# Performance work log

Measured on AMD Instinct MI355X. Metric: run time of the kernel, lower is better.

Reference implementation:

```python
import jax, jax.numpy as jnp
import numpy as np


def _hippo_scale_params(N, L):
    """Replicates HiPPOScale.__init__ for discretization='bilinear' (pure numpy)."""
    q = np.arange(N, dtype=np.float64)
    col, row = np.meshgrid(q, q)
    r = 2 * q + 1
    M = -(np.where(row >= col, r, 0) - np.diag(q))
    T = np.sqrt(np.diag(2 * q + 1))
    A = T @ M @ np.linalg.inv(T)          # (N, N)
    B = np.diag(T)                         # (N,)
    ts = np.arange(1, L + 1, dtype=np.float64)[:, None, None]  # (L,1,1)
    At = A[None] / ts                      # A / t, batched over t
    I = np.eye(N, dtype=np.float64)
    Mm = I[None] - 0.5 * At
    Nn = I[None] + 0.5 * At
    A_stacked = np.linalg.solve(Mm, Nn)                      # (L, N, N)
    Bt = B[None, :] / ts[:, 0, :]                             # (L, N)
    B_stacked = np.linalg.solve(Mm, Bt[..., None])[..., 0]    # (L, N)
    return A_stacked.astype(np.float32), B_stacked.astype(np.float32)


def setup_inputs() -> dict:
    N, L, Bsz = 64, 4096, 64
    key = jax.random.key(0)
    A_st, B_st = _hippo_scale_params(N, L)
    inputs = jax.random.normal(key, (L, Bsz), dtype=jnp.float32)
    return {
        "inputs": inputs,                       # (L, B)
        "A_stacked": jnp.asarray(A_st),         # (L, N, N)
        "B_stacked": jnp.asarray(B_st),         # (L, N)
    }


def reference(inputs, A_stacked, B_stacked):
    # u[t, b, :] = inputs[t, b] * B_stacked[t, :]   -> (L, B, N)
    u = inputs[..., None] * B_stacked[:, None, :]

    # x[t] = A[t] @ x[t-1] + u[t], x[-1] = 0  (time-varying linear recurrence).
    # The torch code computes this via a divide-and-conquer unroll; here we use
    # the equivalent parallel associative scan with elements (A, u) and
    # composition (A2@A1, A2@u1 + u2).
    def combine(e1, e2):
        a1, u1 = e1
        a2, u2 = e2
        a = jnp.matmul(a2, a1)                                  # (l, N, N)
        v = jnp.einsum('...ij,...bj->...bi', a2, u1) + u2       # (l, B, N)
        return (a, v)

    _, x = jax.lax.associative_scan(combine, (A_stacked, u))
    return x  # (L, B, N)
```

## Files before the change

kernel.cpp:

```cpp
#include <hip/hip_runtime.h>
#include <hip/hip_bf16.h>

#define TL 4096
#define NB 64
#define CH 8
#define CN 512
#define AS 72

typedef __attribute__((ext_vector_type(8))) short short8;
typedef __attribute__((ext_vector_type(4))) short short4v;
typedef __attribute__((ext_vector_type(4))) float floatx4;
typedef __attribute__((ext_vector_type(4))) unsigned int uint4v;

__device__ inline floatx4 mfma_bf16(short8 a, short8 b, floatx4 c) {
    return __builtin_amdgcn_mfma_f32_16x16x32_bf16(a, b, c, 0, 0, 0);
}
__device__ inline short bf16_rne(float x) {
    union { __hip_bfloat16 b; unsigned short s; } u;
    u.b = __float2bfloat16(x);
    return (short)u.s;
}
__device__ inline void split_bf16(float x, short& h, short& l) {
    h = bf16_rne(x);
    union { unsigned u; float f; } hv; hv.u = ((unsigned)(unsigned short)h) << 16;
    l = bf16_rne(x - hv.f);
}
__device__ inline void cvt_frag(float4 a, float4 b, short8& H, short8& L) {
    float v[8] = {a.x,a.y,a.z,a.w,b.x,b.y,b.z,b.w};
#pragma unroll
    for (int r = 0; r < 8; ++r) { short hh,ll; split_bf16(v[r],hh,ll); H[r]=hh; L[r]=ll; }
}
__device__ inline void unpack_frag(uint4v a, uint4v b, short8& H, short8& L) {
#pragma unroll
    for (int r = 0; r < 4; ++r) {
        H[r]   = (short)(a[r] >> 16); L[r]   = (short)(a[r] & 0xFFFFu);
        H[4+r] = (short)(b[r] >> 16); L[4+r] = (short)(b[r] & 0xFFFFu);
    }
}

__global__ __launch_bounds__(256, 2)
void hippo_phase1(const float* __restrict__ inp, const float* __restrict__ Ag,
                  const float* __restrict__ Bst,
                  unsigned* __restrict__ P32, float* __restrict__ VT)
{
    __shared__ short SBh[2][NB][AS], SBl[2][NB][AS];
    __shared__ short VBh[2][NB][AS], VBl[2][NB][AS];

    const int tid = threadIdx.x;
    const int c = blockIdx.x, t0 = c * CH;
    const int w = tid >> 6, lane = tid & 63;
    const int quad = lane >> 4, l15 = lane & 15;
    const int arow = 16*w + l15;
    const int wr0  = 16*w + 4*quad;

    float4 rA[2][2];
#pragma unroll
    for (int kc = 0; kc < 2; ++kc) {
        const float* p = Ag + (size_t)(t0+1)*4096 + (size_t)arow*64 + 32*kc + 8*quad;
        rA[kc][0] = *(const float4*)p;
        rA[kc][1] = *(const float4*)(p + 4);
    }
    float4 bnxt = *(const float4*)(Bst + (size_t)(t0+1)*64 + wr0);
    float inxt[4];
#pragma unroll
    for (int ni = 0; ni < 4; ++ni) inxt[ni] = inp[(size_t)(t0+1)*64 + l15 + 16*ni];

    floatx4 accS[4], accV[4];
    {
        const float* A0 = Ag + (size_t)t0 * 4096;
        float4 b0 = *(const float4*)(Bst + (size_t)t0*64 + wr0);
        float bc[4] = {b0.x,b0.y,b0.z,b0.w};
#pragma unroll
        for (int ni = 0; ni < 4; ++ni) {
            const float ii = inp[(size_t)t0*64 + l15 + 16*ni];
#pragma unroll
            for (int r = 0; r < 4; ++r) {
                accS[ni][r] = A0[(size_t)(wr0 + r)*64 + l15 + 16*ni];
                accV[ni][r] = bc[r] * ii;
            }
        }
    }
#pragma unroll
    for (int ni = 0; ni < 4; ++ni) {
        const int cc = l15 + 16*ni;
        short4v h4, l4;
#pragma unroll
        for (int r = 0; r < 4; ++r) { short hh,ll; split_bf16(accS[ni][r],hh,ll); h4[r]=hh; l4[r]=ll; }
        *(short4v*)&SBh[0][cc][wr0] = h4; *(short4v*)&SBl[0][cc][wr0] = l4;
#pragma unroll
        for (int r = 0; r < 4; ++r) { short hh,ll; split_bf16(accV[ni][r],hh,ll); h4[r]=hh; l4[r]=ll; }
        *(short4v*)&VBh[0][cc][wr0] = h4; *(short4v*)&VBl[0][cc][wr0] = l4;
    }
    __syncthreads();

    short8 aH[2], aL[2];
#pragma unroll
    for (int kc = 0; kc < 2; ++kc) cvt_frag(rA[kc][0], rA[kc][1], aH[kc], aL[kc]);

    int cur = 0;
    float4 bcur = bnxt;
    float icur[4];
#pragma unroll
    for (int ni = 0; ni < 4; ++ni) icur[ni] = inxt[ni];

    for (int s = 1; s < CH; ++s) {
        if (s + 1 < CH) {
            const int t1 = t0 + s + 1;
#pragma unroll
            for (int kc = 0; kc < 2; ++kc) {
                const float* p = Ag + (size_t)t1*4096 + (size_t)arow*64 + 32*kc + 8*quad;
                rA[kc][0] = *(const float4*)p;
                rA[kc][1] = *(const float4*)(p + 4);
            }
            bnxt = *(const float4*)(Bst + (size_t)t1*64 + wr0);
#pragma unroll
            for (int ni = 0; ni < 4; ++ni) inxt[ni] = inp[(size_t)t1*64 + l15 + 16*ni];
        }
        {
            float bc[4] = {bcur.x,bcur.y,bcur.z,bcur.w};
#pragma unroll
            for (int ni = 0; ni < 4; ++ni)
#pragma unroll
            for (int r = 0; r < 4; ++r) {
                accS[ni][r] = 0.0f;
                accV[ni][r] = bc[r] * icur[ni];
            }
        }
#pragma unroll
        for (int kc = 0; kc < 2; ++kc) {
            const int ko = 32*kc + 8*quad;
#pragma unroll
            for (int ni = 0; ni < 4; ++ni) {
                const int n = l15 + 16*ni;
                short8 sH = *(const short8*)&SBh[cur][n][ko];
                short8 sL = *(const short8*)&SBl[cur][n][ko];
                short8 vH = *(const short8*)&VBh[cur][n][ko];
                short8 vL = *(const short8*)&VBl[cur][n][ko];
                accS[ni] = mfma_bf16(aH[kc], sH, accS[ni]);
                accS[ni] = mfma_bf16(aH[kc], sL, accS[ni]);
                accS[ni] = mfma_bf16(aL[kc], sH, accS[ni]);
                accV[ni] = mfma_bf16(aH[kc], vH, accV[ni]);
                accV[ni] = mfma_bf16(aH[kc], vL, accV[ni]);
                accV[ni] = mfma_bf16(aL[kc], vH, accV[ni]);
            }
        }
        if (s + 1 < CH) {
#pragma unroll
            for (int kc = 0; kc < 2; ++kc) cvt_frag(rA[kc][0], rA[kc][1], aH[kc], aL[kc]);
            const int nb = cur ^ 1;
#pragma unroll
            for (int ni = 0; ni < 4; ++ni) {
                const int cc = l15 + 16*ni;
                short4v h4, l4;
#pragma unroll
                for (int r = 0; r < 4; ++r) { short hh,ll; split_bf16(accS[ni][r],hh,ll); h4[r]=hh; l4[r]=ll; }
                *(short4v*)&SBh[nb][cc][wr0] = h4; *(short4v*)&SBl[nb][cc][wr0] = l4;
#pragma unroll
                for (int r = 0; r < 4; ++r) { short hh,ll; split_bf16(accV[ni][r],hh,ll); h4[r]=hh; l4[r]=ll; }
                *(short4v*)&VBh[nb][cc][wr0] = h4; *(short4v*)&VBl[nb][cc][wr0] = l4;
            }
            __syncthreads();
            cur ^= 1;
        }
        bcur = bnxt;
#pragma unroll
        for (int ni = 0; ni < 4; ++ni) icur[ni] = inxt[ni];
    }

    unsigned* po = P32 + (size_t)c * 4096;
#pragma unroll
    for (int ni = 0; ni < 4; ++ni) {
        const int cc = l15 + 16*ni;
        *(floatx4*)(VT + (size_t)c*4096 + cc*64 + wr0) = accV[ni];
#pragma unroll
        for (int r = 0; r < 4; ++r) {
            short hh, ll; split_bf16(accS[ni][r], hh, ll);
            po[(size_t)(wr0 + r)*64 + cc] = ((unsigned)(unsigned short)hh << 16) | (unsigned)(unsigned short)ll;
        }
    }
}

__global__ __launch_bounds__(256, 2)
void hippo_seqscan(unsigned* __restrict__ P32, float* __restrict__ VT,
                   int bstride, int off0, int estride)
{
    __shared__ short PBh[2][NB][AS], PBl[2][NB][AS];
    __shared__ short VBh[2][NB][AS], VBl[2][NB][AS];

    const int tid = threadIdx.x;
    const int base = blockIdx.x * bstride + off0;
    const int w = tid >> 6, lane = tid & 63;
    const int quad = lane >> 4, l15 = lane & 15;
    const int arow = 16*w + l15;
    const int wr0  = 16*w + 4*quad;

    {
        const unsigned* p0 = P32 + (size_t)base * 4096;
        const float*    v0 = VT  + (size_t)base * 4096;
#pragma unroll
        for (int q = 0; q < 4; ++q) {
            int f = tid + q * 256;
            int k = f & 63, m0 = (f >> 6) * 4;
            uint4v pk = *(const uint4v*)(p0 + k * 64 + m0);
#pragma unroll
            for (int r = 0; r < 4; ++r) {
                PBh[0][m0 + r][k] = (short)(pk[r] >> 16);
                PBl[0][m0 + r][k] = (short)(pk[r] & 0xFFFFu);
            }
        }
#pragma unroll
        for (int q = 0; q < 4; ++q) {
            int f = tid + q * 256;
            int n = f >> 4, k0 = (f & 15) * 4;
            float4 vv = *(const float4*)(v0 + n * 64 + k0);
            float va[4] = {vv.x, vv.y, vv.z, vv.w};
            short4v vh4, vl4;
#pragma unroll
            for (int r = 0; r < 4; ++r) { short hh, ll; split_bf16(va[r], hh, ll); vh4[r]=hh; vl4[r]=ll; }
            *(short4v*)&VBh[0][n][k0] = vh4; *(short4v*)&VBl[0][n][k0] = vl4;
        }
    }
    uint4v rP[2][2]; float4 preV[4];
    {
        const unsigned* pc = P32 + (size_t)(base + estride) * 4096;
        const float*    vc = VT  + (size_t)(base + estride) * 4096;
#pragma unroll
        for (int kc = 0; kc < 2; ++kc) {
            const unsigned* p = pc + (size_t)arow*64 + 32*kc + 8*quad;
            rP[kc][0] = *(const uint4v*)p;
            rP[kc][1] = *(const uint4v*)(p + 4);
        }
#pragma unroll
        for (int ni = 0; ni < 4; ++ni)
            preV[ni] = *(const float4*)(vc + (size_t)(l15 + 16*ni)*64 + wr0);
    }
    __syncthreads();

    short8 aH[2], aL[2];
#pragma unroll
    for (int kc = 0; kc < 2; ++kc) unpack_frag(rP[kc][0], rP[kc][1], aH[kc], aL[kc]);

    int cur = 0;
    for (int i = 1; i < 8; ++i) {
        const int idx = base + i * estride;
        floatx4 accP[4], accV[4];
#pragma unroll
        for (int ni = 0; ni < 4; ++ni) {
            accV[ni][0] = preV[ni].x; accV[ni][1] = preV[ni].y;
            accV[ni][2] = preV[ni].z; accV[ni][3] = preV[ni].w;
            accP[ni][0]=accP[ni][1]=accP[ni][2]=accP[ni][3]=0.0f;
        }
        if (i + 1 < 8) {
            const unsigned* pc = P32 + (size_t)(base + (i+1) * estride) * 4096;
            const float*    vc = VT  + (size_t)(base + (i+1) * estride) * 4096;
#pragma unroll
            for (int kc = 0; kc < 2; ++kc) {
                const unsigned* p = pc + (size_t)arow*64 + 32*kc + 8*quad;
                rP[kc][0] = *(const uint4v*)p;
                rP[kc][1] = *(const uint4v*)(p + 4);
            }
#pragma unroll
            for (int ni = 0; ni < 4; ++ni)
                preV[ni] = *(const float4*)(vc + (size_t)(l15 + 16*ni)*64 + wr0);
        }
#pragma unroll
        for (int kc = 0; kc < 2; ++kc) {
            const int ko = 32*kc + 8*quad;
#pragma unroll
            for (int ni = 0; ni < 4; ++ni) {
                const int n = l15 + 16*ni;
                short8 pH = *(const short8*)&PBh[cur][n][ko];
                short8 pL = *(const short8*)&PBl[cur][n][ko];
                short8 vH = *(const short8*)&VBh[cur][n][ko];
                short8 vL = *(const short8*)&VBl[cur][n][ko];
                accP[ni] = mfma_bf16(aH[kc], pH, accP[ni]);
                accP[ni] = mfma_bf16(aH[kc], pL, accP[ni]);
                accP[ni] = mfma_bf16(aL[kc], pH, accP[ni]);
                accV[ni] = mfma_bf16(aH[kc], vH, accV[ni]);
                accV[ni] = mfma_bf16(aH[kc], vL, accV[ni]);
                accV[ni] = mfma_bf16(aL[kc], vH, accV[ni]);
            }
        }
        if (i + 1 < 8) {
#pragma unroll
            for (int kc = 0; kc < 2; ++kc) unpack_frag(rP[kc][0], rP[kc][1], aH[kc], aL[kc]);
        }
        unsigned* po = P32 + (size_t)idx * 4096;
        const int nb = cur ^ 1;
#pragma unroll
        for (int ni = 0; ni < 4; ++ni) {
            const int cc = l15 + 16*ni;
            *(floatx4*)(VT + (size_t)idx*4096 + cc*64 + wr0) = accV[ni];
            short4v h4, l4;
#pragma unroll
            for (int r = 0; r < 4; ++r) {
                short hh, ll; split_bf16(accP[ni][r], hh, ll);
                po[(size_t)(wr0+r)*64 + cc] = ((unsigned)(unsigned short)hh << 16) | (unsigned)(unsigned short)ll;
                h4[r]=hh; l4[r]=ll;
            }
            if (i + 1 < 8) {
                *(short4v*)&PBh[nb][cc][wr0] = h4; *(short4v*)&PBl[nb][cc][wr0] = l4;
                short4v vh4, vl4;
#pragma unroll
                for (int r = 0; r < 4; ++r) { short hh,ll; split_bf16(accV[ni][r],hh,ll); vh4[r]=hh; vl4[r]=ll; }
                *(short4v*)&VBh[nb][cc][wr0] = vh4; *(short4v*)&VBl[nb][cc][wr0] = vl4;
            }
        }
        if (i + 1 < 8) __syncthreads();
        cur ^= 1;
    }
}

__global__ __launch_bounds__(256, 2)
void hippo_s3(unsigned* __restrict__ P32, const float* __restrict__ VT)
{
    __shared__ short EBh[2][NB][AS], EBl[2][NB][AS];
    const int tid = threadIdx.x;
    const int w = tid >> 6, lane = tid & 63, quad = lane >> 4, l15 = lane & 15;
    const int arow = 16*w + l15;
    const int wr0  = 16*w + 4*quad;

#pragma unroll
    for (int q = 0; q < 16; ++q) {
        int f = tid + q * 256; EBh[0][f >> 6][f & 63] = 0; EBl[0][f >> 6][f & 63] = 0;
    }
    uint4v rP[2][2]; float4 preV[4];
    {
        const unsigned* pc = P32 + (size_t)63 * 4096;
        const float*    vc = VT  + (size_t)63 * 4096;
#pragma unroll
        for (int kc = 0; kc < 2; ++kc) {
            const unsigned* p = pc + (size_t)arow*64 + 32*kc + 8*quad;
            rP[kc][0] = *(const uint4v*)p;
            rP[kc][1] = *(const uint4v*)(p + 4);
        }
#pragma unroll
        for (int ni = 0; ni < 4; ++ni)
            preV[ni] = *(const float4*)(vc + (size_t)(l15 + 16*ni)*64 + wr0);
    }
    __syncthreads();

    short8 aH[2], aL[2];
#pragma unroll
    for (int kc = 0; kc < 2; ++kc) unpack_frag(rP[kc][0], rP[kc][1], aH[kc], aL[kc]);

    int cur = 0;
    for (int s = 0; s < 7; ++s) {
        const int idx = 64 * s + 63;
        floatx4 acc[4];
#pragma unroll
        for (int ni = 0; ni < 4; ++ni) {
            acc[ni][0] = preV[ni].x; acc[ni][1] = preV[ni].y;
            acc[ni][2] = preV[ni].z; acc[ni][3] = preV[ni].w;
        }
        if (s + 1 < 7) {
            const int idx2 = 64 * (s + 1) + 63;
            const unsigned* pc = P32 + (size_t)idx2 * 4096;
            const float*    vc = VT  + (size_t)idx2 * 4096;
#pragma unroll
            for (int kc = 0; kc < 2; ++kc) {
                const unsigned* p = pc + (size_t)arow*64 + 32*kc + 8*quad;
                rP[kc][0] = *(const uint4v*)p;
                rP[kc][1] = *(const uint4v*)(p + 4);
            }
#pragma unroll
            for (int ni = 0; ni < 4; ++ni)
                preV[ni] = *(const float4*)(vc + (size_t)(l15 + 16*ni)*64 + wr0);
        }
#pragma unroll
        for (int kc = 0; kc < 2; ++kc) {
            const int ko = 32*kc + 8*quad;
#pragma unroll
            for (int ni = 0; ni < 4; ++ni) {
                const int n = l15 + 16*ni;
                short8 eH = *(const short8*)&EBh[cur][n][ko];
                short8 eL = *(const short8*)&EBl[cur][n][ko];
                acc[ni] = mfma_bf16(aH[kc], eH, acc[ni]);
                acc[ni] = mfma_bf16(aH[kc], eL, acc[ni]);
                acc[ni] = mfma_bf16(aL[kc], eH, acc[ni]);
            }
        }
        if (s + 1 < 7) {
#pragma unroll
            for (int kc = 0; kc < 2; ++kc) unpack_frag(rP[kc][0], rP[kc][1], aH[kc], aL[kc]);
        }
        float* eo = (float*)(P32 + (size_t)idx * 4096);
        const int nb = cur ^ 1;
#pragma unroll
        for (int ni = 0; ni < 4; ++ni) {
            const int cc = l15 + 16*ni;
            *(floatx4*)(eo + cc*64 + wr0) = acc[ni];
            if (s + 1 < 7) {
                short4v h4, l4;
#pragma unroll
                for (int r = 0; r < 4; ++r) { short hh,ll; split_bf16(acc[ni][r],hh,ll); h4[r]=hh; l4[r]=ll; }
                *(short4v*)&EBh[nb][cc][wr0] = h4; *(short4v*)&EBl[nb][cc][wr0] = l4;
            }
        }
        if (s + 1 < 7) __syncthreads();
        cur ^= 1;
    }
}

__global__ __launch_bounds__(256, 2)
void hippo_phase3(const float* __restrict__ inp, const float* __restrict__ Ag,
                  const float* __restrict__ Bst, const unsigned* __restrict__ P32,
                  const float* __restrict__ VT, float* __restrict__ out)
{
    __shared__ short XBh[2][NB][AS], XBl[2][NB][AS];

    const int tid = threadIdx.x, c = blockIdx.x, t0 = c * CH;
    const int w = tid >> 6, lane = tid & 63, quad = lane >> 4, l15 = lane & 15;
    const int arow = 16*w + l15;
    const int wr0  = 16*w + 4*quad;
    const int sup = c >> 6, g = c >> 3, gi = g & 7, j = c & 7;

    float4 rA[2][2];
#pragma unroll
    for (int kc = 0; kc < 2; ++kc) {
        const float* p = Ag + (size_t)t0*4096 + (size_t)arow*64 + 32*kc + 8*quad;
        rA[kc][0] = *(const float4*)p;
        rA[kc][1] = *(const float4*)(p + 4);
    }
    float4 bcur = *(const float4*)(Bst + (size_t)t0*64 + wr0);
    float icur[4];
#pragma unroll
    for (int ni = 0; ni < 4; ++ni) icur[ni] = inp[(size_t)t0*64 + l15 + 16*ni];

    if (sup == 0) {
#pragma unroll
        for (int q = 0; q < 16; ++q) { int f = tid + q*256; XBh[0][f>>6][f&63] = 0; XBl[0][f>>6][f&63] = 0; }
    } else {
        const float* e = (const float*)(P32 + (size_t)(64*(sup-1) + 63) * 4096);
#pragma unroll
        for (int q = 0; q < 4; ++q) {
            int f = tid + q*256; int b = f>>4, k0 = (f&15)*4;
            float4 v = *(const float4*)(e + b*64 + k0);
            float va[4] = {v.x,v.y,v.z,v.w};
            short4v h4, l4;
#pragma unroll
            for (int r=0;r<4;++r){short hh,ll;split_bf16(va[r],hh,ll);h4[r]=hh;l4[r]=ll;}
            *(short4v*)&XBh[0][b][k0] = h4; *(short4v*)&XBl[0][b][k0] = l4;
        }
    }
    __syncthreads();
    int cur = 0;

    auto combine = [&](int idx) {
        uint4v rP[2][2];
        const unsigned* pc = P32 + (size_t)idx * 4096;
        const float*    vc = VT  + (size_t)idx * 4096;
#pragma unroll
        for (int kc = 0; kc < 2; ++kc) {
            const unsigned* p = pc + (size_t)arow*64 + 32*kc + 8*quad;
            rP[kc][0] = *(const uint4v*)p;
            rP[kc][1] = *(const uint4v*)(p + 4);
        }
        floatx4 acc[4];
#pragma unroll
        for (int ni = 0; ni < 4; ++ni) {
            float4 vv = *(const float4*)(vc + (size_t)(l15 + 16*ni)*64 + wr0);
            acc[ni][0]=vv.x; acc[ni][1]=vv.y; acc[ni][2]=vv.z; acc[ni][3]=vv.w;
        }
        short8 cH[2], cL[2];
#pragma unroll
        for (int kc = 0; kc < 2; ++kc) unpack_frag(rP[kc][0], rP[kc][1], cH[kc], cL[kc]);
#pragma unroll
        for (int kc = 0; kc < 2; ++kc) {
            const int ko = 32*kc + 8*quad;
#pragma unroll
            for (int ni = 0; ni < 4; ++ni) {
                const int n = l15 + 16*ni;
                short8 xH = *(const short8*)&XBh[cur][n][ko];
                short8 xL = *(const short8*)&XBl[cur][n][ko];
                acc[ni] = mfma_bf16(cH[kc], xH, acc[ni]);
                acc[ni] = mfma_bf16(cH[kc], xL, acc[ni]);
                acc[ni] = mfma_bf16(cL[kc], xH, acc[ni]);
            }
        }
        const int nb = cur ^ 1;
#pragma unroll
        for (int ni = 0; ni < 4; ++ni) {
            const int cc = l15 + 16*ni;
            short4v h4, l4;
#pragma unroll
            for (int r=0;r<4;++r){short hh,ll;split_bf16(acc[ni][r],hh,ll);h4[r]=hh;l4[r]=ll;}
            *(short4v*)&XBh[nb][cc][wr0] = h4; *(short4v*)&XBl[nb][cc][wr0] = l4;
        }
        __syncthreads();
        cur ^= 1;
    };
    if (gi) combine(8*g - 1);
    if (j)  combine(c - 1);

    short8 aH[2], aL[2];
#pragma unroll
    for (int kc = 0; kc < 2; ++kc) cvt_frag(rA[kc][0], rA[kc][1], aH[kc], aL[kc]);

    float4 bnxt; float inxt[4];
    floatx4 acc[4];
    for (int s = 0; s < CH; ++s) {
        const int t = t0 + s;
        if (s + 1 < CH) {
            const int t1 = t + 1;
#pragma unroll
            for (int kc = 0; kc < 2; ++kc) {
                const float* p = Ag + (size_t)t1*4096 + (size_t)arow*64 + 32*kc + 8*quad;
                rA[kc][0] = *(const float4*)p;
                rA[kc][1] = *(const float4*)(p + 4);
            }
            bnxt = *(const float4*)(Bst + (size_t)t1*64 + wr0);
#pragma unroll
            for (int ni = 0; ni < 4; ++ni) inxt[ni] = inp[(size_t)t1*64 + l15 + 16*ni];
        }
        {
            float bc[4] = {bcur.x,bcur.y,bcur.z,bcur.w};
#pragma unroll
            for (int ni=0;ni<4;++ni)
#pragma unroll
            for (int r=0;r<4;++r) acc[ni][r] = bc[r] * icur[ni];
        }
#pragma unroll
        for (int kc = 0; kc < 2; ++kc) {
            const int ko = 32*kc + 8*quad;
#pragma unroll
            for (int ni = 0; ni < 4; ++ni) {
                const int n = l15 + 16*ni;
                short8 xH = *(const short8*)&XBh[cur][n][ko];
                short8 xL = *(const short8*)&XBl[cur][n][ko];
                acc[ni] = mfma_bf16(aH[kc], xH, acc[ni]);
                acc[ni] = mfma_bf16(aH[kc], xL, acc[ni]);
                acc[ni] = mfma_bf16(aL[kc], xH, acc[ni]);
            }
        }
        if (s + 1 < CH) {
#pragma unroll
            for (int kc = 0; kc < 2; ++kc) cvt_frag(rA[kc][0], rA[kc][1], aH[kc], aL[kc]);
        }
        const int nb = cur ^ 1;
#pragma unroll
        for (int ni = 0; ni < 4; ++ni) {
            const int cc = l15 + 16*ni;
            *(floatx4*)(out + (size_t)t*4096 + cc*64 + wr0) = acc[ni];
            if (s + 1 < CH) {
                short4v h4, l4;
#pragma unroll
                for (int r=0;r<4;++r){short hh,ll;split_bf16(acc[ni][r],hh,ll);h4[r]=hh;l4[r]=ll;}
                *(short4v*)&XBh[nb][cc][wr0] = h4; *(short4v*)&XBl[nb][cc][wr0] = l4;
            }
        }
        if (s + 1 < CH) { __syncthreads(); cur ^= 1; }
        bcur = bnxt;
#pragma unroll
        for (int ni = 0; ni < 4; ++ni) icur[ni] = inxt[ni];
    }
}

extern "C" void kernel_launch(void* const* d_in, const int* in_sizes, int n_in,
                              void* d_out, int out_size, void* d_ws, size_t ws_size,
                              hipStream_t stream)
{
    const float* inp = (const float*)d_in[0];
    const float* A   = (const float*)d_in[1];
    const float* Bst = (const float*)d_in[2];
    float* out = (float*)d_out;
    float* ws  = (float*)d_ws;

    unsigned* P32 = (unsigned*)ws;
    float*    VT  = ws + (size_t)CN * 4096;

    hippo_phase1<<<CN, 256, 0, stream>>>(inp, A, Bst, P32, VT);
    hippo_seqscan<<<64, 256, 0, stream>>>(P32, VT, 8, 0, 1);
    hippo_seqscan<<<8, 256, 0, stream>>>(P32, VT, 64, 7, 8);
    hippo_s3<<<1, 256, 0, stream>>>(P32, VT);
    hippo_phase3<<<CN, 256, 0, stream>>>(inp, A, Bst, P32, VT, out);
}
```

Baseline: 183.9 us.

## Fuse five scan kernels into one persistent kernel with grid barriers

Replaces the chain of launches (chunk-local phase, two sequential-scan levels, top-level scan, final expansion) with a single kernel of 512 blocks that synchronise through atomic-counter grid barriers, reusing the same shared-memory buffers across phases. The aim is to remove kernel launch gaps and tail effects between the stages. It depends on all 512 blocks being co-resident (two blocks per CU on 256 CUs), adds a memset for the barrier counters, and leaves most blocks spinning while the small scan stages run.

```diff
diff --git a/kernel.cpp b/kernel.cpp
--- a/kernel.cpp
+++ b/kernel.cpp
@@ -38,13 +38,26 @@
     }
 }
 
+__device__ inline void grid_barrier(unsigned* cnt, unsigned nb) {
+    __threadfence();
+    __syncthreads();
+    if (threadIdx.x == 0) {
+        __hip_atomic_fetch_add(cnt, 1u, __ATOMIC_ACQ_REL, __HIP_MEMORY_SCOPE_AGENT);
+        while (__hip_atomic_load(cnt, __ATOMIC_ACQUIRE, __HIP_MEMORY_SCOPE_AGENT) < nb)
+            __builtin_amdgcn_s_sleep(2);
+    }
+    __syncthreads();
+    __threadfence();
+}
+
 __global__ __launch_bounds__(256, 2)
-void hippo_phase1(const float* __restrict__ inp, const float* __restrict__ Ag,
-                  const float* __restrict__ Bst,
-                  unsigned* __restrict__ P32, float* __restrict__ VT)
+void hippo_fused(const float* __restrict__ inp, const float* __restrict__ Ag,
+                 const float* __restrict__ Bst, unsigned* __restrict__ P32,
+                 float* __restrict__ VT, float* __restrict__ out,
+                 unsigned* __restrict__ gbar)
 {
-    __shared__ short SBh[2][NB][AS], SBl[2][NB][AS];
-    __shared__ short VBh[2][NB][AS], VBl[2][NB][AS];
+    __shared__ short B0h[2][NB][AS], B0l[2][NB][AS];
+    __shared__ short B1h[2][NB][AS], B1l[2][NB][AS];
 
     const int tid = threadIdx.x;
     const int c = blockIdx.x, t0 = c * CH;
@@ -53,206 +66,179 @@
     const int arow = 16*w + l15;
     const int wr0  = 16*w + 4*quad;
 
-    float4 rA[2][2];
+    {
+        float4 rA[2][2];
+#pragma unroll
+        for (int kc = 0; kc < 2; ++kc) {
+            const float* p = Ag + (size_t)(t0+1)*4096 + (size_t)arow*64 + 32*kc + 8*quad;
+            rA[kc][0] = *(const float4*)p;
+            rA[kc][1] = *(const float4*)(p + 4);
+        }
+        float4 bnxt = *(const float4*)(Bst + (size_t)(t0+1)*64 + wr0);
+        float inxt[4];
+#pragma unroll
+        for (int ni = 0; ni < 4; ++ni) inxt[ni] = inp[(size_t)(t0+1)*64 + l15 + 16*ni];
+
+        floatx4 accS[4], accV[4];
+        {
+            const float* A0 = Ag + (size_t)t0 * 4096;
+            float4 b0 = *(const float4*)(Bst + (size_t)t0*64 + wr0);
+            float bc[4] = {b0.x,b0.y,b0.z,b0.w};
+#pragma unroll
+            for (int ni = 0; ni < 4; ++ni) {
+                const float ii = inp[(size_t)t0*64 + l15 + 16*ni];
+#pragma unroll
+                for (int r = 0; r < 4; ++r) {
+                    accS[ni][r] = A0[(size_t)(wr0 + r)*64 + l15 + 16*ni];
+                    accV[ni][r] = bc[r] * ii;
+                }
+            }
+        }
+#pragma unroll
+        for (int ni = 0; ni < 4; ++ni) {
+            const int cc = l15 + 16*ni;
+            short4v h4, l4;
+#pragma unroll
+            for (int r = 0; r < 4; ++r) { short hh,ll; split_bf16(accS[ni][r],hh,ll); h4[r]=hh; l4[r]=ll; }
+            *(short4v*)&B0h[0][cc][wr0] = h4; *(short4v*)&B0l[0][cc][wr0] = l4;
+#pragma unroll
+            for (int r = 0; r < 4; ++r) { short hh,ll; split_bf16(accV[ni][r],hh,ll); h4[r]=hh; l4[r]=ll; }
+            *(short4v*)&B1h[0][cc][wr0] = h4; *(short4v*)&B1l[0][cc][wr0] = l4;
+        }
+        __syncthreads();
+
+        short8 aH[2], aL[2];
+#pragma unroll
+        for (int kc = 0; kc < 2; ++kc) cvt_frag(rA[kc][0], rA[kc][1], aH[kc], aL[kc]);
+
+        int cur = 0;
+        float4 bcur = bnxt;
+        float icur[4];
+#pragma unroll
+        for (int ni = 0; ni < 4; ++ni) icur[ni] = inxt[ni];
+
+        for (int s = 1; s < CH; ++s) {
+            if (s + 1 < CH) {
+                const int t1 = t0 + s + 1;
+#pragma unroll
+                for (int kc = 0; kc < 2; ++kc) {
+                    const float* p = Ag + (size_t)t1*4096 + (size_t)arow*64 + 32*kc + 8*quad;
+                    rA[kc][0] = *(const float4*)p;
+                    rA[kc][1] = *(const float4*)(p + 4);
+                }
+                bnxt = *(const float4*)(Bst + (size_t)t1*64 + wr0);
+#pragma unroll
+                for (int ni = 0; ni < 4; ++ni) inxt[ni] = inp[(size_t)t1*64 + l15 + 16*ni];
+            }
+            {
+                float bc[4] = {bcur.x,bcur.y,bcur.z,bcur.w};
+#pragma unroll
+                for (int ni = 0; ni < 4; ++ni)
+#pragma unroll
+                for (int r = 0; r < 4; ++r) {
+                    accS[ni][r] = 0.0f;
+                    accV[ni][r] = bc[r] * icur[ni];
+                }
+            }
+#pragma unroll
+            for (int kc = 0; kc < 2; ++kc) {
+                const int ko = 32*kc + 8*quad;
+#pragma unroll
+                for (int ni = 0; ni < 4; ++ni) {
+                    const int n = l15 + 16*ni;
+                    short8 sH = *(const short8*)&B0h[cur][n][ko];
+                    short8 sL = *(const short8*)&B0l[cur][n][ko];
+                    short8 vH = *(const short8*)&B1h[cur][n][ko];
+                    short8 vL = *(const short8*)&B1l[cur][n][ko];
+                    accS[ni] = mfma_bf16(aH[kc], sH, accS[ni]);
+                    accS[ni] = mfma_bf16(aH[kc], sL, accS[ni]);
+                    accS[ni] = mfma_bf16(aL[kc], sH, accS[ni]);
+                    accV[ni] = mfma_bf16(aH[kc], vH, accV[ni]);
+                    accV[ni] = mfma_bf16(aH[kc], vL, accV[ni]);
+                    accV[ni] = mfma_bf16(aL[kc], vH, accV[ni]);
+                }
+            }
+            if (s + 1 < CH) {
+#pragma unroll
+                for (int kc = 0; kc < 2; ++kc) cvt_frag(rA[kc][0], rA[kc][1], aH[kc], aL[kc]);
+                const int nb = cur ^ 1;
+#pragma unroll
+                for (int ni = 0; ni < 4; ++ni) {
+                    const int cc = l15 + 16*ni;
+                    short4v h4, l4;
+#pragma unroll
+                    for (int r = 0; r < 4; ++r) { short hh,ll; split_bf16(accS[ni][r],hh,ll); h4[r]=hh; l4[r]=ll; }
+                    *(short4v*)&B0h[nb][cc][wr0] = h4; *(short4v*)&B0l[nb][cc][wr0] = l4;
+#pragma unroll
+                    for (int r = 0; r < 4; ++r) { short hh,ll; split_bf16(accV[ni][r],hh,ll); h4[r]=hh; l4[r]=ll; }
+                    *(short4v*)&B1h[nb][cc][wr0] = h4; *(short4v*)&B1l[nb][cc][wr0] = l4;
+                }
+                __syncthreads();
+                cur ^= 1;
+            }
+            bcur = bnxt;
+#pragma unroll
+            for (int ni = 0; ni < 4; ++ni) icur[ni] = inxt[ni];
+        }
+
+        unsigned* po = P32 + (size_t)c * 4096;
+#pragma unroll
+        for (int ni = 0; ni < 4; ++ni) {
+            const int cc = l15 + 16*ni;
+            *(floatx4*)(VT + (size_t)c*4096 + cc*64 + wr0) = accV[ni];
+#pragma unroll
+            for (int r = 0; r < 4; ++r) {
+                short hh, ll; split_bf16(accS[ni][r], hh, ll);
+                po[(size_t)(wr0 + r)*64 + cc] = ((unsigned)(unsigned short)hh << 16) | (unsigned)(unsigned short)ll;
+            }
+        }
+    }
+
+    float4 rA3[2][2];
 #pragma unroll
     for (int kc = 0; kc < 2; ++kc) {
-        const float* p = Ag + (size_t)(t0+1)*4096 + (size_t)arow*64 + 32*kc + 8*quad;
-        rA[kc][0] = *(const float4*)p;
-        rA[kc][1] = *(const float4*)(p + 4);
+        const float* p = Ag + (size_t)t0*4096 + (size_t)arow*64 + 32*kc + 8*quad;
+        rA3[kc][0] = *(const float4*)p;
+        rA3[kc][1] = *(const float4*)(p + 4);
     }
-    float4 bnxt = *(const float4*)(Bst + (size_t)(t0+1)*64 + wr0);
-    float inxt[4];
-#pragma unroll
-    for (int ni = 0; ni < 4; ++ni) inxt[ni] = inp[(size_t)(t0+1)*64 + l15 + 16*ni];
-
-    floatx4 accS[4], accV[4];
-    {
-        const float* A0 = Ag + (size_t)t0 * 4096;
-        float4 b0 = *(const float4*)(Bst + (size_t)t0*64 + wr0);
-        float bc[4] = {b0.x,b0.y,b0.z,b0.w};
-#pragma unroll
-        for (int ni = 0; ni < 4; ++ni) {
-            const float ii = inp[(size_t)t0*64 + l15 + 16*ni];
-#pragma unroll
-            for (int r = 0; r < 4; ++r) {
-                accS[ni][r] = A0[(size_t)(wr0 + r)*64 + l15 + 16*ni];
-                accV[ni][r] = bc[r] * ii;
-            }
-        }
-    }
-#pragma unroll
-    for (int ni = 0; ni < 4; ++ni) {
-        const int cc = l15 + 16*ni;
-        short4v h4, l4;
-#pragma unroll
-        for (int r = 0; r < 4; ++r) { short hh,ll; split_bf16(accS[ni][r],hh,ll); h4[r]=hh; l4[r]=ll; }
-        *(short4v*)&SBh[0][cc][wr0] = h4; *(short4v*)&SBl[0][cc][wr0] = l4;
-#pragma unroll
-        for (int r = 0; r < 4; ++r) { short hh,ll; split_bf16(accV[ni][r],hh,ll); h4[r]=hh; l4[r]=ll; }
-        *(short4v*)&VBh[0][cc][wr0] = h4; *(short4v*)&VBl[0][cc][wr0] = l4;
-    }
-    __syncthreads();
-
-    short8 aH[2], aL[2];
-#pragma unroll
-    for (int kc = 0; kc < 2; ++kc) cvt_frag(rA[kc][0], rA[kc][1], aH[kc], aL[kc]);
-
-    int cur = 0;
-    float4 bcur = bnxt;
-    float icur[4];
-#pragma unroll
-    for (int ni = 0; ni < 4; ++ni) icur[ni] = inxt[ni];
-
-    for (int s = 1; s < CH; ++s) {
-        if (s + 1 < CH) {
-            const int t1 = t0 + s + 1;
-#pragma unroll
-            for (int kc = 0; kc < 2; ++kc) {
-                const float* p = Ag + (size_t)t1*4096 + (size_t)arow*64 + 32*kc + 8*quad;
-                rA[kc][0] = *(const float4*)p;
-                rA[kc][1] = *(const float4*)(p + 4);
-            }
-            bnxt = *(const float4*)(Bst + (size_t)t1*64 + wr0);
-#pragma unroll
-            for (int ni = 0; ni < 4; ++ni) inxt[ni] = inp[(size_t)t1*64 + l15 + 16*ni];
-        }
+    float4 b3 = *(const float4*)(Bst + (size_t)t0*64 + wr0);
+    float i3[4];
+#pragma unroll
+    for (int ni = 0; ni < 4; ++ni) i3[ni] = inp[(size_t)t0*64 + l15 + 16*ni];
+
+    grid_barrier(gbar + 0, CN);
+
+    auto scan8 = [&](int base, int estride) {
         {
-            float bc[4] = {bcur.x,bcur.y,bcur.z,bcur.w};
-#pragma unroll
-            for (int ni = 0; ni < 4; ++ni)
-#pragma unroll
-            for (int r = 0; r < 4; ++r) {
-                accS[ni][r] = 0.0f;
-                accV[ni][r] = bc[r] * icur[ni];
-            }
-        }
-#pragma unroll
-        for (int kc = 0; kc < 2; ++kc) {
-            const int ko = 32*kc + 8*quad;
-#pragma unroll
-            for (int ni = 0; ni < 4; ++ni) {
-                const int n = l15 + 16*ni;
-                short8 sH = *(const short8*)&SBh[cur][n][ko];
-                short8 sL = *(const short8*)&SBl[cur][n][ko];
-                short8 vH = *(const short8*)&VBh[cur][n][ko];
-                short8 vL = *(const short8*)&VBl[cur][n][ko];
-                accS[ni] = mfma_bf16(aH[kc], sH, accS[ni]);
-                accS[ni] = mfma_bf16(aH[kc], sL, accS[ni]);
-                accS[ni] = mfma_bf16(aL[kc], sH, accS[ni]);
-                accV[ni] = mfma_bf16(aH[kc], vH, accV[ni]);
-                accV[ni] = mfma_bf16(aH[kc], vL, accV[ni]);
-                accV[ni] = mfma_bf16(aL[kc], vH, accV[ni]);
-            }
-        }
-        if (s + 1 < CH) {
-#pragma unroll
-            for (int kc = 0; kc < 2; ++kc) cvt_frag(rA[kc][0], rA[kc][1], aH[kc], aL[kc]);
-            const int nb = cur ^ 1;
-#pragma unroll
-            for (int ni = 0; ni < 4; ++ni) {
-                const int cc = l15 + 16*ni;
-                short4v h4, l4;
-#pragma unroll
-                for (int r = 0; r < 4; ++r) { short hh,ll; split_bf16(accS[ni][r],hh,ll); h4[r]=hh; l4[r]=ll; }
-                *(short4v*)&SBh[nb][cc][wr0] = h4; *(short4v*)&SBl[nb][cc][wr0] = l4;
-#pragma unroll
-                for (int r = 0; r < 4; ++r) { short hh,ll; split_bf16(accV[ni][r],hh,ll); h4[r]=hh; l4[r]=ll; }
-                *(short4v*)&VBh[nb][cc][wr0] = h4; *(short4v*)&VBl[nb][cc][wr0] = l4;
-            }
-            __syncthreads();
-            cur ^= 1;
-        }
-        bcur = bnxt;
-#pragma unroll
-        for (int ni = 0; ni < 4; ++ni) icur[ni] = inxt[ni];
-    }
-
-    unsigned* po = P32 + (size_t)c * 4096;
-#pragma unroll
-    for (int ni = 0; ni < 4; ++ni) {
-        const int cc = l15 + 16*ni;
-        *(floatx4*)(VT + (size_t)c*4096 + cc*64 + wr0) = accV[ni];
-#pragma unroll
-        for (int r = 0; r < 4; ++r) {
-            short hh, ll; split_bf16(accS[ni][r], hh, ll);
-            po[(size_t)(wr0 + r)*64 + cc] = ((unsigned)(unsigned short)hh << 16) | (unsigned)(unsigned short)ll;
-        }
-    }
-}
-
-__global__ __launch_bounds__(256, 2)
-void hippo_seqscan(unsigned* __restrict__ P32, float* __restrict__ VT,
-                   int bstride, int off0, int estride)
-{
-    __shared__ short PBh[2][NB][AS], PBl[2][NB][AS];
-    __shared__ short VBh[2][NB][AS], VBl[2][NB][AS];
-
-    const int tid = threadIdx.x;
-    const int base = blockIdx.x * bstride + off0;
-    const int w = tid >> 6, lane = tid & 63;
-    const int quad = lane >> 4, l15 = lane & 15;
-    const int arow = 16*w + l15;
-    const int wr0  = 16*w + 4*quad;
-
-    {
-        const unsigned* p0 = P32 + (size_t)base * 4096;
-        const float*    v0 = VT  + (size_t)base * 4096;
-#pragma unroll
-        for (int q = 0; q < 4; ++q) {
-            int f = tid + q * 256;
-            int k = f & 63, m0 = (f >> 6) * 4;
-            uint4v pk = *(const uint4v*)(p0 + k * 64 + m0);
-#pragma unroll
-            for (int r = 0; r < 4; ++r) {
-                PBh[0][m0 + r][k] = (short)(pk[r] >> 16);
-                PBl[0][m0 + r][k] = (short)(pk[r] & 0xFFFFu);
-            }
-        }
-#pragma unroll
-        for (int q = 0; q < 4; ++q) {
-            int f = tid + q * 256;
-            int n = f >> 4, k0 = (f & 15) * 4;
-            float4 vv = *(const float4*)(v0 + n * 64 + k0);
-            float va[4] = {vv.x, vv.y, vv.z, vv.w};
-            short4v vh4, vl4;
-#pragma unroll
-            for (int r = 0; r < 4; ++r) { short hh, ll; split_bf16(va[r], hh, ll); vh4[r]=hh; vl4[r]=ll; }
-            *(short4v*)&VBh[0][n][k0] = vh4; *(short4v*)&VBl[0][n][k0] = vl4;
-        }
-    }
-    uint4v rP[2][2]; float4 preV[4];
-    {
-        const unsigned* pc = P32 + (size_t)(base + estride) * 4096;
-        const float*    vc = VT  + (size_t)(base + estride) * 4096;
-#pragma unroll
-        for (int kc = 0; kc < 2; ++kc) {
-            const unsigned* p = pc + (size_t)arow*64 + 32*kc + 8*quad;
-            rP[kc][0] = *(const uint4v*)p;
-            rP[kc][1] = *(const uint4v*)(p + 4);
-        }
-#pragma unroll
-        for (int ni = 0; ni < 4; ++ni)
-            preV[ni] = *(const float4*)(vc + (size_t)(l15 + 16*ni)*64 + wr0);
-    }
-    __syncthreads();
-
-    short8 aH[2], aL[2];
-#pragma unroll
-    for (int kc = 0; kc < 2; ++kc) unpack_frag(rP[kc][0], rP[kc][1], aH[kc], aL[kc]);
-
-    int cur = 0;
-    for (int i = 1; i < 8; ++i) {
-        const int idx = base + i * estride;
-        floatx4 accP[4], accV[4];
-#pragma unroll
-        for (int ni = 0; ni < 4; ++ni) {
-            accV[ni][0] = preV[ni].x; accV[ni][1] = preV[ni].y;
-            accV[ni][2] = preV[ni].z; accV[ni][3] = preV[ni].w;
-            accP[ni][0]=accP[ni][1]=accP[ni][2]=accP[ni][3]=0.0f;
-        }
-        if (i + 1 < 8) {
-            const unsigned* pc = P32 + (size_t)(base + (i+1) * estride) * 4096;
-            const float*    vc = VT  + (size_t)(base + (i+1) * estride) * 4096;
+            const unsigned* p0 = P32 + (size_t)base * 4096;
+            const float*    v0 = VT  + (size_t)base * 4096;
+#pragma unroll
+            for (int q = 0; q < 4; ++q) {
+                int f = tid + q * 256;
+                int k = f & 63, m0 = (f >> 6) * 4;
+                uint4v pk = *(const uint4v*)(p0 + k * 64 + m0);
+#pragma unroll
+                for (int r = 0; r < 4; ++r) {
+                    B0h[0][m0 + r][k] = (short)(pk[r] >> 16);
+                    B0l[0][m0 + r][k] = (short)(pk[r] & 0xFFFFu);
+                }
+            }
+#pragma unroll
+            for (int q = 0; q < 4; ++q) {
+                int f = tid + q * 256;
+                int n = f >> 4, k0 = (f & 15) * 4;
+                float4 vv = *(const float4*)(v0 + n * 64 + k0);
+                float va[4] = {vv.x, vv.y, vv.z, vv.w};
+                short4v vh4, vl4;
+#pragma unroll
+                for (int r = 0; r < 4; ++r) { short hh, ll; split_bf16(va[r], hh, ll); vh4[r]=hh; vl4[r]=ll; }
+                *(short4v*)&B1h[0][n][k0] = vh4; *(short4v*)&B1l[0][n][k0] = vl4;
+            }
+        }
+        uint4v rP[2][2]; float4 pV[4];
+        {
+            const unsigned* pc = P32 + (size_t)(base + estride) * 4096;
+            const float*    vc = VT  + (size_t)(base + estride) * 4096;
 #pragma unroll
             for (int kc = 0; kc < 2; ++kc) {
                 const unsigned* p = pc + (size_t)arow*64 + 32*kc + 8*quad;
@@ -261,102 +247,99 @@
             }
 #pragma unroll
             for (int ni = 0; ni < 4; ++ni)
-                preV[ni] = *(const float4*)(vc + (size_t)(l15 + 16*ni)*64 + wr0);
-        }
-#pragma unroll
-        for (int kc = 0; kc < 2; ++kc) {
-            const int ko = 32*kc + 8*quad;
-#pragma unroll
-            for (int ni = 0; ni < 4; ++ni) {
-                const int n = l15 + 16*ni;
-                short8 pH = *(const short8*)&PBh[cur][n][ko];
-                short8 pL = *(const short8*)&PBl[cur][n][ko];
-                short8 vH = *(const short8*)&VBh[cur][n][ko];
-                short8 vL = *(const short8*)&VBl[cur][n][ko];
-                accP[ni] = mfma_bf16(aH[kc], pH, accP[ni]);
-                accP[ni] = mfma_bf16(aH[kc], pL, accP[ni]);
-                accP[ni] = mfma_bf16(aL[kc], pH, accP[ni]);
-                accV[ni] = mfma_bf16(aH[kc], vH, accV[ni]);
-                accV[ni] = mfma_bf16(aH[kc], vL, accV[ni]);
-                accV[ni] = mfma_bf16(aL[kc], vH, accV[ni]);
-            }
-        }
-        if (i + 1 < 8) {
-#pragma unroll
-            for (int kc = 0; kc < 2; ++kc) unpack_frag(rP[kc][0], rP[kc][1], aH[kc], aL[kc]);
-        }
-        unsigned* po = P32 + (size_t)idx * 4096;
-        const int nb = cur ^ 1;
-#pragma unroll
-        for (int ni = 0; ni < 4; ++ni) {
-            const int cc = l15 + 16*ni;
-            *(floatx4*)(VT + (size_t)idx*4096 + cc*64 + wr0) = accV[ni];
-            short4v h4, l4;
-#pragma unroll
-            for (int r = 0; r < 4; ++r) {
-                short hh, ll; split_bf16(accP[ni][r], hh, ll);
-                po[(size_t)(wr0+r)*64 + cc] = ((unsigned)(unsigned short)hh << 16) | (unsigned)(unsigned short)ll;
-                h4[r]=hh; l4[r]=ll;
+                pV[ni] = *(const float4*)(vc + (size_t)(l15 + 16*ni)*64 + wr0);
+        }
+        __syncthreads();
+
+        short8 aH[2], aL[2];
+#pragma unroll
+        for (int kc = 0; kc < 2; ++kc) unpack_frag(rP[kc][0], rP[kc][1], aH[kc], aL[kc]);
+
+        int cur = 0;
+        for (int i = 1; i < 8; ++i) {
+            const int idx = base + i * estride;
+            floatx4 accP[4], accV[4];
+#pragma unroll
+            for (int ni = 0; ni < 4; ++ni) {
+                accV[ni][0] = pV[ni].x; accV[ni][1] = pV[ni].y;
+                accV[ni][2] = pV[ni].z; accV[ni][3] = pV[ni].w;
+                accP[ni][0]=accP[ni][1]=accP[ni][2]=accP[ni][3]=0.0f;
             }
             if (i + 1 < 8) {
-                *(short4v*)&PBh[nb][cc][wr0] = h4; *(short4v*)&PBl[nb][cc][wr0] = l4;
-                short4v vh4, vl4;
-#pragma unroll
-                for (int r = 0; r < 4; ++r) { short hh,ll; split_bf16(accV[ni][r],hh,ll); vh4[r]=hh; vl4[r]=ll; }
-                *(short4v*)&VBh[nb][cc][wr0] = vh4; *(short4v*)&VBl[nb][cc][wr0] = vl4;
-            }
-        }
-        if (i + 1 < 8) __syncthreads();
-        cur ^= 1;
-    }
-}
-
-__global__ __launch_bounds__(256, 2)
-void hippo_s3(unsigned* __restrict__ P32, const float* __restrict__ VT)
-{
-    __shared__ short EBh[2][NB][AS], EBl[2][NB][AS];
-    const int tid = threadIdx.x;
-    const int w = tid >> 6, lane = tid & 63, quad = lane >> 4, l15 = lane & 15;
-    const int arow = 16*w + l15;
-    const int wr0  = 16*w + 4*quad;
-
-#pragma unroll
-    for (int q = 0; q < 16; ++q) {
-        int f = tid + q * 256; EBh[0][f >> 6][f & 63] = 0; EBl[0][f >> 6][f & 63] = 0;
-    }
-    uint4v rP[2][2]; float4 preV[4];
-    {
-        const unsigned* pc = P32 + (size_t)63 * 4096;
-        const float*    vc = VT  + (size_t)63 * 4096;
-#pragma unroll
-        for (int kc = 0; kc < 2; ++kc) {
-            const unsigned* p = pc + (size_t)arow*64 + 32*kc + 8*quad;
-            rP[kc][0] = *(const uint4v*)p;
-            rP[kc][1] = *(const uint4v*)(p + 4);
-        }
-#pragma unroll
-        for (int ni = 0; ni < 4; ++ni)
-            preV[ni] = *(const float4*)(vc + (size_t)(l15 + 16*ni)*64 + wr0);
-    }
-    __syncthreads();
-
-    short8 aH[2], aL[2];
-#pragma unroll
-    for (int kc = 0; kc < 2; ++kc) unpack_frag(rP[kc][0], rP[kc][1], aH[kc], aL[kc]);
-
-    int cur = 0;
-    for (int s = 0; s < 7; ++s) {
-        const int idx = 64 * s + 63;
-        floatx4 acc[4];
-#pragma unroll
-        for (int ni = 0; ni < 4; ++ni) {
-            acc[ni][0] = preV[ni].x; acc[ni][1] = preV[ni].y;
-            acc[ni][2] = preV[ni].z; acc[ni][3] = preV[ni].w;
-        }
-        if (s + 1 < 7) {
-            const int idx2 = 64 * (s + 1) + 63;
-            const unsigned* pc = P32 + (size_t)idx2 * 4096;
-            const float*    vc = VT  + (size_t)idx2 * 4096;
+                const unsigned* pc = P32 + (size_t)(base + (i+1) * estride) * 4096;
+                const float*    vc = VT  + (size_t)(base + (i+1) * estride) * 4096;
+#pragma unroll
+                for (int kc = 0; kc < 2; ++kc) {
+                    const unsigned* p = pc + (size_t)arow*64 + 32*kc + 8*quad;
+                    rP[kc][0] = *(const uint4v*)p;
+                    rP[kc][1] = *(const uint4v*)(p + 4);
+                }
+#pragma unroll
+                for (int ni = 0; ni < 4; ++ni)
+                    pV[ni] = *(const float4*)(vc + (size_t)(l15 + 16*ni)*64 + wr0);
+            }
+#pragma unroll
+            for (int kc = 0; kc < 2; ++kc) {
+                const int ko = 32*kc + 8*quad;
+#pragma unroll
+                for (int ni = 0; ni < 4; ++ni) {
+                    const int n = l15 + 16*ni;
+                    short8 pH = *(const short8*)&B0h[cur][n][ko];
+                    short8 pL = *(const short8*)&B0l[cur][n][ko];
+                    short8 vH = *(const short8*)&B1h[cur][n][ko];
+                    short8 vL = *(const short8*)&B1l[cur][n][ko];
+                    accP[ni] = mfma_bf16(aH[kc], pH, accP[ni]);
+                    accP[ni] = mfma_bf16(aH[kc], pL, accP[ni]);
+                    accP[ni] = mfma_bf16(aL[kc], pH, accP[ni]);
+                    accV[ni] = mfma_bf16(aH[kc], vH, accV[ni]);
+                    accV[ni] = mfma_bf16(aH[kc], vL, accV[ni]);
+                    accV[ni] = mfma_bf16(aL[kc], vH, accV[ni]);
+                }
+            }
+            if (i + 1 < 8) {
+#pragma unroll
+                for (int kc = 0; kc < 2; ++kc) unpack_frag(rP[kc][0], rP[kc][1], aH[kc], aL[kc]);
+            }
+            unsigned* po = P32 + (size_t)idx * 4096;
+            const int nb = cur ^ 1;
+#pragma unroll
+            for (int ni = 0; ni < 4; ++ni) {
+                const int cc = l15 + 16*ni;
+                *(floatx4*)(VT + (size_t)idx*4096 + cc*64 + wr0) = accV[ni];
+                short4v h4, l4;
+#pragma unroll
+                for (int r = 0; r < 4; ++r) {
+                    short hh, ll; split_bf16(accP[ni][r], hh, ll);
+                    po[(size_t)(wr0+r)*64 + cc] = ((unsigned)(unsigned short)hh << 16) | (unsigned)(unsigned short)ll;
+                    h4[r]=hh; l4[r]=ll;
+                }
+                if (i + 1 < 8) {
+                    *(short4v*)&B0h[nb][cc][wr0] = h4; *(short4v*)&B0l[nb][cc][wr0] = l4;
+                    short4v vh4, vl4;
+#pragma unroll
+                    for (int r = 0; r < 4; ++r) { short hh,ll; split_bf16(accV[ni][r],hh,ll); vh4[r]=hh; vl4[r]=ll; }
+                    *(short4v*)&B1h[nb][cc][wr0] = vh4; *(short4v*)&B1l[nb][cc][wr0] = vl4;
+                }
+            }
+            if (i + 1 < 8) __syncthreads();
+            cur ^= 1;
+        }
+    };
+
+    if (c < 64) scan8(c * 8, 1);
+    grid_barrier(gbar + 1, CN);
+    if (c < 8) scan8(64 * c + 7, 8);
+    grid_barrier(gbar + 2, CN);
+
+    if (c == 0) {
+#pragma unroll
+        for (int q = 0; q < 16; ++q) {
+            int f = tid + q * 256; B0h[0][f >> 6][f & 63] = 0; B0l[0][f >> 6][f & 63] = 0;
+        }
+        uint4v rP[2][2]; float4 pV[4];
+        {
+            const unsigned* pc = P32 + (size_t)63 * 4096;
+            const float*    vc = VT  + (size_t)63 * 4096;
 #pragma unroll
             for (int kc = 0; kc < 2; ++kc) {
                 const unsigned* p = pc + (size_t)arow*64 + 32*kc + 8*quad;
@@ -365,194 +348,208 @@
             }
 #pragma unroll
             for (int ni = 0; ni < 4; ++ni)
-                preV[ni] = *(const float4*)(vc + (size_t)(l15 + 16*ni)*64 + wr0);
-        }
-#pragma unroll
-        for (int kc = 0; kc < 2; ++kc) {
-            const int ko = 32*kc + 8*quad;
-#pragma unroll
-            for (int ni = 0; ni < 4; ++ni) {
-                const int n = l15 + 16*ni;
-                short8 eH = *(const short8*)&EBh[cur][n][ko];
-                short8 eL = *(const short8*)&EBl[cur][n][ko];
-                acc[ni] = mfma_bf16(aH[kc], eH, acc[ni]);
-                acc[ni] = mfma_bf16(aH[kc], eL, acc[ni]);
-                acc[ni] = mfma_bf16(aL[kc], eH, acc[ni]);
-            }
-        }
-        if (s + 1 < 7) {
-#pragma unroll
-            for (int kc = 0; kc < 2; ++kc) unpack_frag(rP[kc][0], rP[kc][1], aH[kc], aL[kc]);
-        }
-        float* eo = (float*)(P32 + (size_t)idx * 4096);
-        const int nb = cur ^ 1;
-#pragma unroll
-        for (int ni = 0; ni < 4; ++ni) {
-            const int cc = l15 + 16*ni;
-            *(floatx4*)(eo + cc*64 + wr0) = acc[ni];
+                pV[ni] = *(const float4*)(vc + (size_t)(l15 + 16*ni)*64 + wr0);
+        }
+        __syncthreads();
+
+        short8 aH[2], aL[2];
+#pragma unroll
+        for (int kc = 0; kc < 2; ++kc) unpack_frag(rP[kc][0], rP[kc][1], aH[kc], aL[kc]);
+
+        int cur = 0;
+        for (int s = 0; s < 7; ++s) {
+            const int idx = 64 * s + 63;
+            floatx4 acc[4];
+#pragma unroll
+            for (int ni = 0; ni < 4; ++ni) {
+                acc[ni][0] = pV[ni].x; acc[ni][1] = pV[ni].y;
+                acc[ni][2] = pV[ni].z; acc[ni][3] = pV[ni].w;
+            }
             if (s + 1 < 7) {
+                const int idx2 = 64 * (s + 1) + 63;
+                const unsigned* pc = P32 + (size_t)idx2 * 4096;
+                const float*    vc = VT  + (size_t)idx2 * 4096;
+#pragma unroll
+                for (int kc = 0; kc < 2; ++kc) {
+                    const unsigned* p = pc + (size_t)arow*64 + 32*kc + 8*quad;
+                    rP[kc][0] = *(const uint4v*)p;
+                    rP[kc][1] = *(const uint4v*)(p + 4);
+                }
+#pragma unroll
+                for (int ni = 0; ni < 4; ++ni)
+                    pV[ni] = *(const float4*)(vc + (size_t)(l15 + 16*ni)*64 + wr0);
+            }
+#pragma unroll
+            for (int kc = 0; kc < 2; ++kc) {
+                const int ko = 32*kc + 8*quad;
+#pragma unroll
+                for (int ni = 0; ni < 4; ++ni) {
+                    const int n = l15 + 16*ni;
+                    short8 eH = *(const short8*)&B0h[cur][n][ko];
+                    short8 eL = *(const short8*)&B0l[cur][n][ko];
+                    acc[ni] = mfma_bf16(aH[kc], eH, acc[ni]);
+                    acc[ni] = mfma_bf16(aH[kc], eL, acc[ni]);
+                    acc[ni] = mfma_bf16(aL[kc], eH, acc[ni]);
+                }
+            }
+            if (s + 1 < 7) {
+#pragma unroll
+                for (int kc = 0; kc < 2; ++kc) unpack_frag(rP[kc][0], rP[kc][1], aH[kc], aL[kc]);
+            }
+            float* eo = (float*)(P32 + (size_t)idx * 4096);
+            const int nb = cur ^ 1;
+#pragma unroll
+            for (int ni = 0; ni < 4; ++ni) {
+                const int cc = l15 + 16*ni;
+                *(floatx4*)(eo + cc*64 + wr0) = acc[ni];
+                if (s + 1 < 7) {
+                    short4v h4, l4;
+#pragma unroll
+                    for (int r = 0; r < 4; ++r) { short hh,ll; split_bf16(acc[ni][r],hh,ll); h4[r]=hh; l4[r]=ll; }
+                    *(short4v*)&B0h[nb][cc][wr0] = h4; *(short4v*)&B0l[nb][cc][wr0] = l4;
+                }
+            }
+            if (s + 1 < 7) __syncthreads();
+            cur ^= 1;
+        }
+    }
+    grid_barrier(gbar + 3, CN);
+
+    {
+        const int sup = c >> 6, g = c >> 3, gi = g & 7, j = c & 7;
+
+        if (sup == 0) {
+#pragma unroll
+            for (int q = 0; q < 16; ++q) { int f = tid + q*256; B0h[0][f>>6][f&63] = 0; B0l[0][f>>6][f&63] = 0; }
+        } else {
+            const float* e = (const float*)(P32 + (size_t)(64*(sup-1) + 63) * 4096);
+#pragma unroll
+            for (int q = 0; q < 4; ++q) {
+                int f = tid + q*256; int b = f>>4, k0 = (f&15)*4;
+                float4 v = *(const float4*)(e + b*64 + k0);
+                float va[4] = {v.x,v.y,v.z,v.w};
                 short4v h4, l4;
 #pragma unroll
-                for (int r = 0; r < 4; ++r) { short hh,ll; split_bf16(acc[ni][r],hh,ll); h4[r]=hh; l4[r]=ll; }
-                *(short4v*)&EBh[nb][cc][wr0] = h4; *(short4v*)&EBl[nb][cc][wr0] = l4;
-            }
-        }
-        if (s + 1 < 7) __syncthreads();
-        cur ^= 1;
-    }
-}
-
-__global__ __launch_bounds__(256, 2)
-void hippo_phase3(const float* __restrict__ inp, const float* __restrict__ Ag,
-                  const float* __restrict__ Bst, const unsigned* __restrict__ P32,
-                  const float* __restrict__ VT, float* __restrict__ out)
-{
-    __shared__ short XBh[2][NB][AS], XBl[2][NB][AS];
-
-    const int tid = threadIdx.x, c = blockIdx.x, t0 = c * CH;
-    const int w = tid >> 6, lane = tid & 63, quad = lane >> 4, l15 = lane & 15;
-    const int arow = 16*w + l15;
-    const int wr0  = 16*w + 4*quad;
-    const int sup = c >> 6, g = c >> 3, gi = g & 7, j = c & 7;
-
-    float4 rA[2][2];
-#pragma unroll
-    for (int kc = 0; kc < 2; ++kc) {
-        const float* p = Ag + (size_t)t0*4096 + (size_t)arow*64 + 32*kc + 8*quad;
-        rA[kc][0] = *(const float4*)p;
-        rA[kc][1] = *(const float4*)(p + 4);
-    }
-    float4 bcur = *(const float4*)(Bst + (size_t)t0*64 + wr0);
-    float icur[4];
-#pragma unroll
-    for (int ni = 0; ni < 4; ++ni) icur[ni] = inp[(size_t)t0*64 + l15 + 16*ni];
-
-    if (sup == 0) {
-#pragma unroll
-        for (int q = 0; q < 16; ++q) { int f = tid + q*256; XBh[0][f>>6][f&63] = 0; XBl[0][f>>6][f&63] = 0; }
-    } else {
-        const float* e = (const float*)(P32 + (size_t)(64*(sup-1) + 63) * 4096);
-#pragma unroll
-        for (int q = 0; q < 4; ++q) {
-            int f = tid + q*256; int b = f>>4, k0 = (f&15)*4;
-            float4 v = *(const float4*)(e + b*64 + k0);
-            float va[4] = {v.x,v.y,v.z,v.w};
-            short4v h4, l4;
-#pragma unroll
-            for (int r=0;r<4;++r){short hh,ll;split_bf16(va[r],hh,ll);h4[r]=hh;l4[r]=ll;}
-            *(short4v*)&XBh[0][b][k0] = h4; *(short4v*)&XBl[0][b][k0] = l4;
-        }
-    }
-    __syncthreads();
-    int cur = 0;
-
-    auto combine = [&](int idx) {
-        uint4v rP[2][2];
-        const unsigned* pc = P32 + (size_t)idx * 4096;
-        const float*    vc = VT  + (size_t)idx * 4096;
-#pragma unroll
-        for (int kc = 0; kc < 2; ++kc) {
-            const unsigned* p = pc + (size_t)arow*64 + 32*kc + 8*quad;
-            rP[kc][0] = *(const uint4v*)p;
-            rP[kc][1] = *(const uint4v*)(p + 4);
-        }
+                for (int r=0;r<4;++r){short hh,ll;split_bf16(va[r],hh,ll);h4[r]=hh;l4[r]=ll;}
+                *(short4v*)&B0h[0][b][k0] = h4; *(short4v*)&B0l[0][b][k0] = l4;
+            }
+        }
+        __syncthreads();
+        int cur = 0;
+
+        auto combine = [&](int idx) {
+            uint4v rP[2][2];
+            const unsigned* pc = P32 + (size_t)idx * 4096;
+            const float*    vc = VT  + (size_t)idx * 4096;
+#pragma unroll
+            for (int kc = 0; kc < 2; ++kc) {
+                const unsigned* p = pc + (size_t)arow*64 + 32*kc + 8*quad;
+                rP[kc][0] = *(const uint4v*)p;
+                rP[kc][1] = *(const uint4v*)(p + 4);
+            }
+            floatx4 acc[4];
+#pragma unroll
+            for (int ni = 0; ni < 4; ++ni) {
+                float4 vv = *(const float4*)(vc + (size_t)(l15 + 16*ni)*64 + wr0);
+                acc[ni][0]=vv.x; acc[ni][1]=vv.y; acc[ni][2]=vv.z; acc[ni][3]=vv.w;
+            }
+            short8 cH[2], cL[2];
+#pragma unroll
+            for (int kc = 0; kc < 2; ++kc) unpack_frag(rP[kc][0], rP[kc][1], cH[kc], cL[kc]);
+#pragma unroll
+            for (int kc = 0; kc < 2; ++kc) {
+                const int ko = 32*kc + 8*quad;
+#pragma unroll
+                for (int ni = 0; ni < 4; ++ni) {
+                    const int n = l15 + 16*ni;
+                    short8 xH = *(const short8*)&B0h[cur][n][ko];
+                    short8 xL = *(const short8*)&B0l[cur][n][ko];
+                    acc[ni] = mfma_bf16(cH[kc], xH, acc[ni]);
+                    acc[ni] = mfma_bf16(cH[kc], xL, acc[ni]);
+                    acc[ni] = mfma_bf16(cL[kc], xH, acc[ni]);
+                }
+            }
+            const int nb = cur ^ 1;
+#pragma unroll
+            for (int ni = 0; ni < 4; ++ni) {
+                const int cc = l15 + 16*ni;
+                short4v h4, l4;
+#pragma unroll
+                for (int r=0;r<4;++r){short hh,ll;split_bf16(acc[ni][r],hh,ll);h4[r]=hh;l4[r]=ll;}
+                *(short4v*)&B0h[nb][cc][wr0] = h4; *(short4v*)&B0l[nb][cc][wr0] = l4;
+            }
+            __syncthreads();
+            cur ^= 1;
+        };
+        if (gi) combine(8*g - 1);
+        if (j)  combine(c - 1);
+
+        short8 aH[2], aL[2];
+#pragma unroll
+        for (int kc = 0; kc < 2; ++kc) cvt_frag(rA3[kc][0], rA3[kc][1], aH[kc], aL[kc]);
+
+        float4 rA[2][2];
+        float4 bcur = b3, bnxt;
+        float icur[4], inxt[4];
+#pragma unroll
+        for (int ni = 0; ni < 4; ++ni) icur[ni] = i3[ni];
+
         floatx4 acc[4];
-#pragma unroll
-        for (int ni = 0; ni < 4; ++ni) {
-            float4 vv = *(const float4*)(vc + (size_t)(l15 + 16*ni)*64 + wr0);
-            acc[ni][0]=vv.x; acc[ni][1]=vv.y; acc[ni][2]=vv.z; acc[ni][3]=vv.w;
-        }
-        short8 cH[2], cL[2];
-#pragma unroll
-        for (int kc = 0; kc < 2; ++kc) unpack_frag(rP[kc][0], rP[kc][1], cH[kc], cL[kc]);
-#pragma unroll
-        for (int kc = 0; kc < 2; ++kc) {
-            const int ko = 32*kc + 8*quad;
-#pragma unroll
-            for (int ni = 0; ni < 4; ++ni) {
-                const int n = l15 + 16*ni;
-                short8 xH = *(const short8*)&XBh[cur][n][ko];
-                short8 xL = *(const short8*)&XBl[cur][n][ko];
-                acc[ni] = mfma_bf16(cH[kc], xH, acc[ni]);
-                acc[ni] = mfma_bf16(cH[kc], xL, acc[ni]);
-                acc[ni] = mfma_bf16(cL[kc], xH, acc[ni]);
-            }
-        }
-        const int nb = cur ^ 1;
-#pragma unroll
-        for (int ni = 0; ni < 4; ++ni) {
-            const int cc = l15 + 16*ni;
-            short4v h4, l4;
-#pragma unroll
-            for (int r=0;r<4;++r){short hh,ll;split_bf16(acc[ni][r],hh,ll);h4[r]=hh;l4[r]=ll;}
-            *(short4v*)&XBh[nb][cc][wr0] = h4; *(short4v*)&XBl[nb][cc][wr0] = l4;
-        }
-        __syncthreads();
-        cur ^= 1;
-    };
-    if (gi) combine(8*g - 1);
-    if (j)  combine(c - 1);
-
-    short8 aH[2], aL[2];
-#pragma unroll
-    for (int kc = 0; kc < 2; ++kc) cvt_frag(rA[kc][0], rA[kc][1], aH[kc], aL[kc]);
-
-    float4 bnxt; float inxt[4];
-    floatx4 acc[4];
-    for (int s = 0; s < CH; ++s) {
-        const int t = t0 + s;
-        if (s + 1 < CH) {
-            const int t1 = t + 1;
-#pragma unroll
-            for (int kc = 0; kc < 2; ++kc) {
-                const float* p = Ag + (size_t)t1*4096 + (size_t)arow*64 + 32*kc + 8*quad;
-                rA[kc][0] = *(const float4*)p;
-                rA[kc][1] = *(const float4*)(p + 4);
-            }
-            bnxt = *(const float4*)(Bst + (size_t)t1*64 + wr0);
-#pragma unroll
-            for (int ni = 0; ni < 4; ++ni) inxt[ni] = inp[(size_t)t1*64 + l15 + 16*ni];
-        }
-        {
-            float bc[4] = {bcur.x,bcur.y,bcur.z,bcur.w};
-#pragma unroll
-            for (int ni=0;ni<4;++ni)
-#pragma unroll
-            for (int r=0;r<4;++r) acc[ni][r] = bc[r] * icur[ni];
-        }
-#pragma unroll
-        for (int kc = 0; kc < 2; ++kc) {
-            const int ko = 32*kc + 8*quad;
-#pragma unroll
-            for (int ni = 0; ni < 4; ++ni) {
-                const int n = l15 + 16*ni;
-                short8 xH = *(const short8*)&XBh[cur][n][ko];
-                short8 xL = *(const short8*)&XBl[cur][n][ko];
-                acc[ni] = mfma_bf16(aH[kc], xH, acc[ni]);
-                acc[ni] = mfma_bf16(aH[kc], xL, acc[ni]);
-                acc[ni] = mfma_bf16(aL[kc], xH, acc[ni]);
-            }
-        }
-        if (s + 1 < CH) {
-#pragma unroll
-            for (int kc = 0; kc < 2; ++kc) cvt_frag(rA[kc][0], rA[kc][1], aH[kc], aL[kc]);
-        }
-        const int nb = cur ^ 1;
-#pragma unroll
-        for (int ni = 0; ni < 4; ++ni) {
-            const int cc = l15 + 16*ni;
-            *(floatx4*)(out + (size_t)t*4096 + cc*64 + wr0) = acc[ni];
+        for (int s = 0; s < CH; ++s) {
+            const int t = t0 + s;
             if (s + 1 < CH) {
-                short4v h4, l4;
-#pragma unroll
-                for (int r=0;r<4;++r){short hh,ll;split_bf16(acc[ni][r],hh,ll);h4[r]=hh;l4[r]=ll;}
-                *(short4v*)&XBh[nb][cc][wr0] = h4; *(short4v*)&XBl[nb][cc][wr0] = l4;
-            }
-        }
-        if (s + 1 < CH) { __syncthreads(); cur ^= 1; }
-        bcur = bnxt;
-#pragma unroll
-        for (int ni = 0; ni < 4; ++ni) icur[ni] = inxt[ni];
+                const int t1 = t + 1;
+#pragma unroll
+                for (int kc = 0; kc < 2; ++kc) {
+                    const float* p = Ag + (size_t)t1*4096 + (size_t)arow*64 + 32*kc + 8*quad;
+                    rA[kc][0] = *(const float4*)p;
+                    rA[kc][1] = *(const float4*)(p + 4);
+                }
+                bnxt = *(const float4*)(Bst + (size_t)t1*64 + wr0);
+#pragma unroll
+                for (int ni = 0; ni < 4; ++ni) inxt[ni] = inp[(size_t)t1*64 + l15 + 16*ni];
+            }
+            {
+                float bc[4] = {bcur.x,bcur.y,bcur.z,bcur.w};
+#pragma unroll
+                for (int ni=0;ni<4;++ni)
+#pragma unroll
+                for (int r=0;r<4;++r) acc[ni][r] = bc[r] * icur[ni];
+            }
+#pragma unroll
+            for (int kc = 0; kc < 2; ++kc) {
+                const int ko = 32*kc + 8*quad;
+#pragma unroll
+                for (int ni = 0; ni < 4; ++ni) {
+                    const int n = l15 + 16*ni;
+                    short8 xH = *(const short8*)&B0h[cur][n][ko];
+                    short8 xL = *(const short8*)&B0l[cur][n][ko];
+                    acc[ni] = mfma_bf16(aH[kc], xH, acc[ni]);
+                    acc[ni] = mfma_bf16(aH[kc], xL, acc[ni]);
+                    acc[ni] = mfma_bf16(aL[kc], xH, acc[ni]);
+                }
+            }
+            if (s + 1 < CH) {
+#pragma unroll
+                for (int kc = 0; kc < 2; ++kc) cvt_frag(rA[kc][0], rA[kc][1], aH[kc], aL[kc]);
+            }
+            const int nb = cur ^ 1;
+#pragma unroll
+            for (int ni = 0; ni < 4; ++ni) {
+                const int cc = l15 + 16*ni;
+                *(floatx4*)(out + (size_t)t*4096 + cc*64 + wr0) = acc[ni];
+                if (s + 1 < CH) {
+                    short4v h4, l4;
+#pragma unroll
+                    for (int r=0;r<4;++r){short hh,ll;split_bf16(acc[ni][r],hh,ll);h4[r]=hh;l4[r]=ll;}
+                    *(short4v*)&B0h[nb][cc][wr0] = h4; *(short4v*)&B0l[nb][cc][wr0] = l4;
+                }
+            }
+            if (s + 1 < CH) { __syncthreads(); cur ^= 1; }
+            bcur = bnxt;
+#pragma unroll
+            for (int ni = 0; ni < 4; ++ni) icur[ni] = inxt[ni];
+        }
     }
 }
 
@@ -567,11 +564,9 @@
     float* ws  = (float*)d_ws;
 
     unsigned* P32 = (unsigned*)ws;
-    float*    VT  = ws + (size_t)CN * 4096;
-
-    hippo_phase1<<<CN, 256, 0, stream>>>(inp, A, Bst, P32, VT);
-    hippo_seqscan<<<64, 256, 0, stream>>>(P32, VT, 8, 0, 1);
-    hippo_seqscan<<<8, 256, 0, stream>>>(P32, VT, 64, 7, 8);
-    hippo_s3<<<1, 256, 0, stream>>>(P32, VT);
-    hippo_phase3<<<CN, 256, 0, stream>>>(inp, A, Bst, P32, VT, out);
-}
+    float*    VT  = (float*)ws + (size_t)CN * 4096;
+    unsigned* gbar = (unsigned*)((char*)d_ws + (size_t)16 * 1024 * 1024);
+
+    hipMemsetAsync(gbar, 0, 4 * sizeof(unsigned), stream);
+    hippo_fused<<<CN, 256, 0, stream>>>(inp, A, Bst, P32, VT, out, gbar);
+}
```

Result: slower. 728.1 us (+295.9%).
